# Performance work log

Hardware: AMD Instinct MI355X
Metric: run time of the kernel (lower is better)

The kernel has to match this reference:

```python
import jax, jax.numpy as jnp
import numpy as np

N, F, H, D = 4096, 512, 4, 64        # nodes, in features, heads, per-head dim
HID, OUT, NCLS, E = 1024, 256, 40, 65536  # FFN hidden, GAT dim, classes, edges
EPS = 1e-5


def _bn(x, g, b):
    # BatchNorm1d with batch statistics (training-mode math, biased variance)
    m = x.mean(axis=0)
    v = jnp.var(x, axis=0)
    return (x - m) * jax.lax.rsqrt(v + EPS) * g + b


def _ffn(x, g1, b1, W1, c1, g2, b2, W2, c2):
    x = jax.nn.gelu(_bn(x, g1, b1) @ W1.T + c1, approximate=False)
    x = jax.nn.gelu(_bn(x, g2, b2) @ W2.T + c2, approximate=False)
    return x


def setup_inputs() -> dict:
    key = jax.random.key(0)
    ks = jax.random.split(key, 12)
    nrm = lambda k, shape: jax.random.normal(k, shape, jnp.float32) * 0.05
    node_features = jax.random.normal(ks[0], (N, F), jnp.float32)
    edges = jax.random.randint(ks[1], (2, E), 0, N)
    adj = jnp.eye(N, dtype=bool)  # self loops, as in __init__
    adj = adj.at[edges[0], edges[1]].set(True)
    adj = adj.at[edges[1], edges[0]].set(True)
    return dict(
        node_features=node_features,
        pre_g1=jnp.ones(F), pre_b1=jnp.zeros(F),
        pre_W1=nrm(ks[2], (HID, F)), pre_c1=jnp.zeros(HID),
        pre_g2=jnp.ones(HID), pre_b2=jnp.zeros(HID),
        pre_W2=nrm(ks[3], (OUT, HID)), pre_c2=jnp.zeros(OUT),
        Wp=nrm(ks[4], (H * D, OUT)),           # GAT preprocess Linear, no bias
        Wa=nrm(ks[5], (2 * D,)),               # attention Linear(2d -> 1), no bias
        ln_g=jnp.ones(OUT), ln_b=jnp.zeros(OUT),
        post_g1=jnp.ones(OUT), post_b1=jnp.zeros(OUT),
        post_W1=nrm(ks[6], (HID, OUT)), post_c1=jnp.zeros(HID),
        post_g2=jnp.ones(HID), post_b2=jnp.zeros(HID),
        post_W2=nrm(ks[7], (OUT, HID)), post_c2=jnp.zeros(OUT),
        Wl=nrm(ks[8], (NCLS, OUT)), cl=jnp.zeros(NCLS),
        adjacency=adj,
        input_node_indices=jax.random.randint(ks[9], (8192,), 0, N),
    )


def reference(node_features, pre_g1, pre_b1, pre_W1, pre_c1, pre_g2, pre_b2,
              pre_W2, pre_c2, Wp, Wa, ln_g, ln_b, post_g1, post_b1, post_W1,
              post_c1, post_g2, post_b2, post_W2, post_c2, Wl, cl,
              adjacency, input_node_indices):
    # preprocess FFN: [N,F] -> [N,OUT]
    x = _ffn(node_features, pre_g1, pre_b1, pre_W1, pre_c1,
             pre_g2, pre_b2, pre_W2, pre_c2)
    # GAT layer
    xh = (x @ Wp.T).reshape(N, H, D)
    # cat([x_source, x_target]) @ Wa == x[j] . Wa[:D] + x[i] . Wa[D:]
    a_src = jnp.einsum('jhd,d->jh', xh, Wa[:D])
    a_tgt = jnp.einsum('ihd,d->ih', xh, Wa[D:])
    e = jax.nn.leaky_relu(a_src[None, :, :] + a_tgt[:, None, :],
                          negative_slope=0.2)          # [i, j, h]
    e = jnp.where(adjacency[:, :, None], e, -jnp.inf)  # masked_fill(~adj, -inf)
    att = jax.nn.softmax(e, axis=1)                    # softmax over neighbors j
    h = jnp.einsum('ijh,jhd->ihd', att, xh).reshape(N, H * D)
    # residual + LayerNorm (dropout disabled for deterministic reference)
    x = x + h
    mu = x.mean(-1, keepdims=True)
    var = jnp.var(x, axis=-1, keepdims=True)
    x = (x - mu) * jax.lax.rsqrt(var + EPS) * ln_g + ln_b
    # postprocess FFN + gather + logits
    x = _ffn(x, post_g1, post_b1, post_W1, post_c1,
             post_g2, post_b2, post_W2, post_c2)
    emb = x[input_node_indices]
    return emb @ Wl.T + cl
```

## Files before the change

### kernel.cpp

```cpp
#include <hip/hip_runtime.h>
#include <hip/hip_bf16.h>


#define NNODES 4096
#define CAP 128

typedef unsigned short u16;
typedef __attribute__((ext_vector_type(8))) short bf16x8;
typedef __attribute__((ext_vector_type(4))) float f32x4;

__device__ __forceinline__ float gelu_f(float x) {
    return 0.5f * x * (1.0f + erff(x * 0.70710678118654752f));
}
__device__ __forceinline__ u16 f2bf(float x) {
    union { float f; unsigned u; } v; v.f = x;
    unsigned r = v.u + 0x7fff + ((v.u >> 16) & 1);
    return (u16)(r >> 16);
}
__device__ __forceinline__ float bf2f(u16 b) {
    return __uint_as_float(((unsigned)b) << 16);
}
__device__ __forceinline__ void gload16(const void* g, void* l) {
    __builtin_amdgcn_global_load_lds(
        (const __attribute__((address_space(1))) unsigned int*)g,
        (__attribute__((address_space(3))) unsigned int*)l, 16, 0, 0);
}

__global__ __launch_bounds__(256) void prep_kernel(
    const unsigned char* __restrict__ adj, int* __restrict__ nbr,
    int* __restrict__ deg, const float* __restrict__ nf,
    float* __restrict__ part, u16* __restrict__ nf16)
{
    __shared__ int lists[4][CAP];
    __shared__ int cnts[4];
    __shared__ int sflag;
    const int t = threadIdx.x;
    const int wv = t >> 6, lane = t & 63;

    if (blockIdx.x >= NNODES) {
        const int bid = blockIdx.x - NNODES;
        const int r0 = bid * 32;
        const int cchunk = t & 127;
        const int rsub = t >> 7;
        float s[4] = {0.f, 0.f, 0.f, 0.f}, q[4] = {0.f, 0.f, 0.f, 0.f};
        for (int r = rsub; r < 32; r += 2) {
            float4 v = *(const float4*)(nf + (size_t)(r0 + r) * 512 + cchunk * 4);
            float vv[4] = {v.x, v.y, v.z, v.w};
            ushort4 o;
            o.x = f2bf(vv[0]); o.y = f2bf(vv[1]);
            o.z = f2bf(vv[2]); o.w = f2bf(vv[3]);
            *(ushort4*)(nf16 + (size_t)(r0 + r) * 512 + cchunk * 4) = o;
#pragma unroll
            for (int j = 0; j < 4; ++j) { s[j] += vv[j]; q[j] += vv[j] * vv[j]; }
        }
        const size_t slice = (size_t)bid * 2 + rsub;
#pragma unroll
        for (int j = 0; j < 4; ++j) {
            int c = cchunk * 4 + j;
            part[(slice * 512 + c) * 2 + 0] = s[j];
            part[(slice * 512 + c) * 2 + 1] = q[j];
        }
        return;
    }

    const int i = blockIdx.x;
    if (wv == 0) {
        bool a = adj[(size_t)lane * 4097] != 0;
        bool b = ((const unsigned int*)adj)[(size_t)lane * 4097] != 0;
        unsigned long long mA = __ballot(a);
        unsigned long long mB = __ballot(b);
        if (lane == 0) sflag = (__popcll(mA) >= __popcll(mB)) ? 0 : 1;
    }
    __syncthreads();
    int cnt = 0;
    if (sflag == 1) {
        const uint4* row = (const uint4*)((const unsigned int*)adj + (size_t)i * NNODES);
#pragma unroll
        for (int w = 0; w < 4; ++w) {
            uint4 v = row[w * 256 + t];
            unsigned wd[4] = {v.x, v.y, v.z, v.w};
#pragma unroll
            for (int j = 0; j < 4; ++j) {
                bool on = wd[j] != 0;
                unsigned long long m = __ballot(on);
                int pre = __popcll(m & ((1ull << lane) - 1ull));
                if (on && cnt + pre < CAP)
                    lists[wv][cnt + pre] = (w * 256 + t) * 4 + j;
                cnt += __popcll(m);
            }
        }
    } else {
        uint4 v = ((const uint4*)(adj + (size_t)i * NNODES))[t];
        unsigned wd[4] = {v.x, v.y, v.z, v.w};
#pragma unroll
        for (int j = 0; j < 4; ++j)
#pragma unroll
            for (int b = 0; b < 4; ++b) {
                bool on = ((wd[j] >> (8 * b)) & 0xffu) != 0;
                unsigned long long m = __ballot(on);
                int pre = __popcll(m & ((1ull << lane) - 1ull));
                if (on && cnt + pre < CAP)
                    lists[wv][cnt + pre] = t * 16 + j * 4 + b;
                cnt += __popcll(m);
            }
    }
    if (lane == 0) cnts[wv] = cnt < CAP ? cnt : CAP;
    __syncthreads();
    int offw = 0;
#pragma unroll
    for (int w2 = 0; w2 < 4; ++w2) if (w2 < wv) offw += cnts[w2];
    int myc = cnts[wv];
    for (int k = lane; k < myc; k += 64) {
        int pos = offw + k;
        if (pos < CAP) nbr[(size_t)i * CAP + pos] = lists[wv][k];
    }
    if (t == 0) {
        int tot = cnts[0] + cnts[1] + cnts[2] + cnts[3];
        deg[i] = tot < CAP ? tot : CAP;
    }
}

__global__ __launch_bounds__(256) void xln_stats(
    const float* __restrict__ X, float* __restrict__ part)
{
    const int bid = blockIdx.x;
    const int r0 = bid * 32;
    const int t = threadIdx.x;
    const int cchunk = t & 63;
    const int rsub = t >> 6;
    float s[4] = {0.f, 0.f, 0.f, 0.f}, q[4] = {0.f, 0.f, 0.f, 0.f};
    for (int r = rsub; r < 32; r += 4) {
        float4 v = *(const float4*)(X + (size_t)(r0 + r) * 256 + cchunk * 4);
        float vv[4] = {v.x, v.y, v.z, v.w};
#pragma unroll
        for (int j = 0; j < 4; ++j) { s[j] += vv[j]; q[j] += vv[j] * vv[j]; }
    }
    const size_t slice = (size_t)bid * 4 + rsub;
#pragma unroll
    for (int j = 0; j < 4; ++j) {
        int c = cchunk * 4 + j;
        part[(slice * 256 + c) * 2 + 0] = s[j];
        part[(slice * 256 + c) * 2 + 1] = q[j];
    }
}

__global__ __launch_bounds__(256) void colstats_final(
    const float* __restrict__ part, const float* __restrict__ g,
    const float* __restrict__ bt, float* __restrict__ scl,
    float* __restrict__ shf, int NB, int C)
{
    __shared__ float sred[16][17];
    __shared__ float qred[16][17];
    const int t = threadIdx.x;
    const int cs = t & 15, grp = t >> 4;
    const int c = blockIdx.x * 16 + cs;
    float s = 0.f, q = 0.f;
    for (int b = grp; b < NB; b += 16) {
        s += part[((size_t)b * C + c) * 2 + 0];
        q += part[((size_t)b * C + c) * 2 + 1];
    }
    sred[grp][cs] = s; qred[grp][cs] = q;
    __syncthreads();
    if (grp == 0) {
        float S = 0.f, Q = 0.f;
#pragma unroll
        for (int j = 0; j < 16; ++j) { S += sred[j][cs]; Q += qred[j][cs]; }
        float m = S * (1.0f / 4096.0f);
        float v = Q * (1.0f / 4096.0f) - m * m;
        float sc = g[c] * rsqrtf(v + 1e-5f);
        scl[c] = sc;
        shf[c] = bt[c] - m * sc;
    }
}

__global__ __launch_bounds__(256) void foldw_kernel(
    const float* __restrict__ W, const float* __restrict__ scl,
    const float* __restrict__ shf, const float* __restrict__ bias,
    u16* __restrict__ W16, float* __restrict__ bout, int K, int nvalid)
{
    __shared__ float red[4];
    const int n = blockIdx.x, t = threadIdx.x;
    u16* o = W16 + (size_t)n * K;
    if (n >= nvalid) {
        for (int k = t; k < K; k += 256) o[k] = 0;
        if (t == 0) bout[n] = 0.f;
        return;
    }
    const float* w = W + (size_t)n * K;
    float part = 0.f;
    for (int k = t; k < K; k += 256) {
        float wv = w[k];
        float s = scl ? scl[k] : 1.f;
        float f = shf ? shf[k] : 0.f;
        o[k] = f2bf(wv * s);
        part += wv * f;
    }
    int lane = t & 63, wv_ = t >> 6;
#pragma unroll
    for (int off = 32; off > 0; off >>= 1) part += __shfl_down(part, off);
    if (lane == 0) red[wv_] = part;
    __syncthreads();
    if (t == 0)
        bout[n] = (bias ? bias[n] : 0.f) + red[0] + red[1] + red[2] + red[3];
}

__global__ __launch_bounds__(256) void foldw2_kernel(
    const float* __restrict__ Wp, const float* __restrict__ Wl,
    const float* __restrict__ cl, u16* __restrict__ Wp16,
    u16* __restrict__ WlP16, float* __restrict__ CLP)
{
    const int n = blockIdx.x, t = threadIdx.x;
    if (n < 256) {
        Wp16[(size_t)n * 256 + t] = f2bf(Wp[(size_t)n * 256 + t]);
    } else {
        int m = n - 256;
        if (m < 40) {
            WlP16[(size_t)m * 256 + t] = f2bf(Wl[(size_t)m * 256 + t]);
            if (t == 0) CLP[m] = cl[m];
        } else {
            WlP16[(size_t)m * 256 + t] = 0;
            if (t == 0) CLP[m] = 0.f;
        }
    }
}

template<bool EPI, bool S16, bool STATS>
__global__ __launch_bounds__(256) void mfma_gemm(
    const u16* __restrict__ A, const u16* __restrict__ W,
    const float* __restrict__ bias, u16* __restrict__ C16,
    float* __restrict__ PART, int M, int N, int K)
{
    __shared__ u16 As[2][4096];
    __shared__ u16 Bs[2][4096];
    __shared__ float ep1[2][64];
    __shared__ float ep2[2][64];
    const int t = threadIdx.x;
    const int lane = t & 63, wv = t >> 6;
    const int wm = (wv >> 1) * 32, wn = (wv & 1) * 32;
    const int tile_m = blockIdx.y * 64, tile_n = blockIdx.x * 64;

    f32x4 acc[2][2];
#pragma unroll
    for (int i = 0; i < 2; ++i)
#pragma unroll
        for (int j = 0; j < 2; ++j)
#pragma unroll
            for (int e = 0; e < 4; ++e) acc[i][j][e] = 0.f;

    int srow[2], soff[2];
#pragma unroll
    for (int i = 0; i < 2; ++i) {
        int f = i * 256 + t;
        srow[i] = f >> 3;
        soff[i] = ((f & 7) ^ (srow[i] & 7)) * 8;
    }
    const int wvoff = wv * 1024;
    const int frow_a0 = wm + (lane & 15);
    const int frow_b0 = wn + (lane & 15);
    const int fk = (lane >> 4) * 16;

    const int NT = K >> 6;
    int cur = 0;

#define STAGE(B, KT)                                                         \
    {                                                                        \
        _Pragma("unroll")                                                    \
        for (int i = 0; i < 2; ++i) {                                        \
            gload16(A + (size_t)(tile_m + srow[i]) * K + (KT) * 64 + soff[i],\
                    (char*)As[B] + wvoff + i * 4096);                        \
            gload16(W + (size_t)(tile_n + srow[i]) * K + (KT) * 64 + soff[i],\
                    (char*)Bs[B] + wvoff + i * 4096);                        \
        }                                                                    \
    }

    STAGE(0, 0);
    __syncthreads();
    for (int kt = 0; kt < NT; ++kt) {
        if (kt + 1 < NT) STAGE(cur ^ 1, kt + 1);
        const char* baseA = (const char*)As[cur];
        const char* baseB = (const char*)Bs[cur];
#pragma unroll
        for (int kk = 0; kk < 2; ++kk) {
            bf16x8 a[2], b[2];
#pragma unroll
            for (int mi = 0; mi < 2; ++mi) {
                int r = frow_a0 + mi * 16;
                a[mi] = *(const bf16x8*)(baseA + r * 128 +
                        ((kk * 64 + fk) ^ ((r & 7) << 4)));
            }
#pragma unroll
            for (int ni = 0; ni < 2; ++ni) {
                int r = frow_b0 + ni * 16;
                b[ni] = *(const bf16x8*)(baseB + r * 128 +
                        ((kk * 64 + fk) ^ ((r & 7) << 4)));
            }
#pragma unroll
            for (int mi = 0; mi < 2; ++mi)
#pragma unroll
                for (int ni = 0; ni < 2; ++ni)
                    acc[mi][ni] = __builtin_amdgcn_mfma_f32_16x16x32_bf16(
                        a[mi], b[ni], acc[mi][ni], 0, 0, 0);
        }
        __syncthreads();
        cur ^= 1;
    }
#undef STAGE

    float st0 = 0.f, st1 = 0.f, sq0 = 0.f, sq1 = 0.f;
#pragma unroll
    for (int mi = 0; mi < 2; ++mi) {
#pragma unroll
        for (int ni = 0; ni < 2; ++ni) {
            int col = tile_n + wn + ni * 16 + (lane & 15);
            float bs = 0.f;
            if (EPI) bs = bias[col];
#pragma unroll
            for (int e = 0; e < 4; ++e) {
                int row = tile_m + wm + mi * 16 + ((lane >> 4) << 2) + e;
                float c = acc[mi][ni][e];
                if (EPI) c = gelu_f(c + bs);
                if (S16) C16[(size_t)row * N + col] = f2bf(c);
                if (STATS) {
                    if (ni == 0) { st0 += c; sq0 += c * c; }
                    else         { st1 += c; sq1 += c * c; }
                }
            }
        }
    }

    if (STATS) {
        float s0 = st0, s1 = st1, q0 = sq0, q1 = sq1;
        s0 += __shfl_xor(s0, 16); s0 += __shfl_xor(s0, 32);
        s1 += __shfl_xor(s1, 16); s1 += __shfl_xor(s1, 32);
        q0 += __shfl_xor(q0, 16); q0 += __shfl_xor(q0, 32);
        q1 += __shfl_xor(q1, 16); q1 += __shfl_xor(q1, 32);
        if (lane < 16) {
            ep1[wv >> 1][wn + lane] = s0;       ep2[wv >> 1][wn + lane] = q0;
            ep1[wv >> 1][wn + 16 + lane] = s1;  ep2[wv >> 1][wn + 16 + lane] = q1;
        }
        __syncthreads();
        if (t < 64) {
            PART[((size_t)blockIdx.y * N + tile_n + t) * 2 + 0] = ep1[0][t] + ep1[1][t];
            PART[((size_t)blockIdx.y * N + tile_n + t) * 2 + 1] = ep2[0][t] + ep2[1][t];
        }
    }
}

template<bool EPI, bool S16, bool ASRCF>
__global__ __launch_bounds__(512) void mfma_gemm8(
    const u16* __restrict__ A, const u16* __restrict__ W,
    const float* __restrict__ bias, u16* __restrict__ C16,
    const float* __restrict__ Wa, float* __restrict__ ASRC,
    float* __restrict__ ATGT, int M, int N, int K)
{
    __shared__ u16 As[2][4096];
    __shared__ u16 Bs[2][4096];
    __shared__ float ep1[2][64];
    __shared__ float ep2[2][64];
    const int t = threadIdx.x;
    const int lane = t & 63, wv = t >> 6;
    const int wm = (wv >> 1) * 16, wn = (wv & 1) * 32;
    const int tile_m = blockIdx.y * 64, tile_n = blockIdx.x * 64;

    f32x4 acc[2];
#pragma unroll
    for (int j = 0; j < 2; ++j)
#pragma unroll
        for (int e = 0; e < 4; ++e) acc[j][e] = 0.f;

    const int srow = t >> 3;
    const int soff = ((t & 7) ^ (srow & 7)) * 8;
    const int wvoff = wv * 1024;
    const int frow_a = wm + (lane & 15);
    const int frow_b0 = wn + (lane & 15);
    const int fk = (lane >> 4) * 16;

    const int NT = K >> 6;
    int cur = 0;

#define STAGE8(B, KT)                                                        \
    {                                                                        \
        gload16(A + (size_t)(tile_m + srow) * K + (KT) * 64 + soff,          \
                (char*)As[B] + wvoff);                                       \
        gload16(W + (size_t)(tile_n + srow) * K + (KT) * 64 + soff,          \
                (char*)Bs[B] + wvoff);                                       \
    }

    STAGE8(0, 0);
    __syncthreads();
    for (int kt = 0; kt < NT; ++kt) {
        if (kt + 1 < NT) STAGE8(cur ^ 1, kt + 1);
        const char* baseA = (const char*)As[cur];
        const char* baseB = (const char*)Bs[cur];
#pragma unroll
        for (int kk = 0; kk < 2; ++kk) {
            bf16x8 a, b[2];
            {
                int r = frow_a;
                a = *(const bf16x8*)(baseA + r * 128 +
                    ((kk * 64 + fk) ^ ((r & 7) << 4)));
            }
#pragma unroll
            for (int ni = 0; ni < 2; ++ni) {
                int r = frow_b0 + ni * 16;
                b[ni] = *(const bf16x8*)(baseB + r * 128 +
                        ((kk * 64 + fk) ^ ((r & 7) << 4)));
            }
#pragma unroll
            for (int ni = 0; ni < 2; ++ni)
                acc[ni] = __builtin_amdgcn_mfma_f32_16x16x32_bf16(
                    a, b[ni], acc[ni], 0, 0, 0);
        }
        __syncthreads();
        cur ^= 1;
    }
#undef STAGE8

#pragma unroll
    for (int ni = 0; ni < 2; ++ni) {
        int col = tile_n + wn + ni * 16 + (lane & 15);
        float bs = 0.f;
        if (EPI) bs = bias[col];
#pragma unroll
        for (int e = 0; e < 4; ++e) {
            int row = tile_m + wm + ((lane >> 4) << 2) + e;
            float c = acc[ni][e];
            if (EPI) c = gelu_f(c + bs);
            if (S16) C16[(size_t)row * N + col] = f2bf(c);
        }
    }

    if (ASRCF) {
        const int cl = lane & 15;
        float ws0 = Wa[wn + cl],      ws1 = Wa[wn + 16 + cl];
        float wt0 = Wa[64 + wn + cl], wt1 = Wa[64 + wn + 16 + cl];
#pragma unroll
        for (int e = 0; e < 4; ++e) {
            float vs = acc[0][e] * ws0 + acc[1][e] * ws1;
            float vt = acc[0][e] * wt0 + acc[1][e] * wt1;
#pragma unroll
            for (int off = 1; off < 16; off <<= 1) {
                vs += __shfl_xor(vs, off);
                vt += __shfl_xor(vt, off);
            }
            if (cl == 0) {
                int row = wm + ((lane >> 4) << 2) + e;
                ep1[wv & 1][row] = vs;
                ep2[wv & 1][row] = vt;
            }
        }
        __syncthreads();
        if (t < 64) {
            int h = blockIdx.x;
            ASRC[(size_t)(tile_m + t) * 4 + h] = ep1[0][t] + ep1[1][t];
            ATGT[(size_t)(tile_m + t) * 4 + h] = ep2[0][t] + ep2[1][t];
        }
    }
}

__global__ __launch_bounds__(512) void logits_mfma(
    const u16* __restrict__ xf16, const int* __restrict__ idxs,
    const u16* __restrict__ WlP, const float* __restrict__ clP,
    float* __restrict__ out)
{
    __shared__ u16 As[2][4096];
    __shared__ u16 Bs[2][4096];
    const int t = threadIdx.x;
    const int lane = t & 63, wv = t >> 6;
    const int wm = (wv >> 1) * 16, wn = (wv & 1) * 32;
    const int tile_m = blockIdx.x * 64;

    f32x4 acc[2];
#pragma unroll
    for (int j = 0; j < 2; ++j)
#pragma unroll
        for (int e = 0; e < 4; ++e) acc[j][e] = 0.f;

    const int srow = t >> 3;
    const int soff = ((t & 7) ^ (srow & 7)) * 8;
    const int gr = idxs[tile_m + srow];
    const int wvoff = wv * 1024;
    const int frow_a = wm + (lane & 15);
    const int frow_b0 = wn + (lane & 15);
    const int fk = (lane >> 4) * 16;

#define LSTAGE8(B, KT)                                                       \
    {                                                                        \
        gload16(xf16 + (size_t)gr * 256 + (KT) * 64 + soff,                  \
                (char*)As[B] + wvoff);                                       \
        gload16(WlP + (size_t)srow * 256 + (KT) * 64 + soff,                 \
                (char*)Bs[B] + wvoff);                                       \
    }

    int cur = 0;
    LSTAGE8(0, 0);
    __syncthreads();
#pragma unroll
    for (int kt = 0; kt < 4; ++kt) {
        if (kt + 1 < 4) LSTAGE8(cur ^ 1, kt + 1);
        const char* baseA = (const char*)As[cur];
        const char* baseB = (const char*)Bs[cur];
#pragma unroll
        for (int kk = 0; kk < 2; ++kk) {
            bf16x8 a, b[2];
            {
                int r = frow_a;
                a = *(const bf16x8*)(baseA + r * 128 +
                    ((kk * 64 + fk) ^ ((r & 7) << 4)));
            }
#pragma unroll
            for (int ni = 0; ni < 2; ++ni) {
                int r = frow_b0 + ni * 16;
                b[ni] = *(const bf16x8*)(baseB + r * 128 +
                        ((kk * 64 + fk) ^ ((r & 7) << 4)));
            }
#pragma unroll
            for (int ni = 0; ni < 2; ++ni)
                acc[ni] = __builtin_amdgcn_mfma_f32_16x16x32_bf16(
                    a, b[ni], acc[ni], 0, 0, 0);
        }
        __syncthreads();
        cur ^= 1;
    }
#undef LSTAGE8

#pragma unroll
    for (int ni = 0; ni < 2; ++ni) {
        int col = wn + ni * 16 + (lane & 15);
        if (col < 40) {
            float bs = clP[col];
#pragma unroll
            for (int e = 0; e < 4; ++e) {
                int row = tile_m + wm + ((lane >> 4) << 2) + e;
                out[(size_t)row * 40 + col] = acc[ni][e] + bs;
            }
        }
    }
}

__global__ __launch_bounds__(256) void attn_ln_kernel(
    const u16* __restrict__ xh, const u16* __restrict__ x0,
    const float* __restrict__ asrc, const float* __restrict__ atgt,
    const int* __restrict__ nbr, const int* __restrict__ deg_,
    const float* __restrict__ ln_g, const float* __restrict__ ln_b,
    float* __restrict__ xln32, u16* __restrict__ xln16)
{
    __shared__ float att[CAP * 4];
    __shared__ int nb[CAP];
    __shared__ float red[8];
    const int i = blockIdx.x;
    const int t = threadIdx.x;
    const int wv = t >> 6, lane = t & 63;
    const int dg = deg_[i];

    for (int k = t; k < dg; k += 256) nb[k] = nbr[(size_t)i * CAP + k];
    __syncthreads();

    for (int idx = t; idx < dg * 4; idx += 256) {
        int k = idx >> 2, h = idx & 3;
        float e = asrc[nb[k] * 4 + h] + atgt[i * 4 + h];
        att[idx] = e > 0.f ? e : 0.2f * e;
    }
    __syncthreads();

    {
        const int h = wv;
        float m = -1e30f;
        for (int k = lane; k < dg; k += 64) m = fmaxf(m, att[k * 4 + h]);
#pragma unroll
        for (int off = 32; off > 0; off >>= 1) m = fmaxf(m, __shfl_xor(m, off));
        float s = 0.f;
        for (int k = lane; k < dg; k += 64) s += expf(att[k * 4 + h] - m);
#pragma unroll
        for (int off = 32; off > 0; off >>= 1) s += __shfl_xor(s, off);
        float inv = 1.0f / s;
        for (int k = lane; k < dg; k += 64)
            att[k * 4 + h] = expf(att[k * 4 + h] - m) * inv;
    }

    const int h = wv;
    float acc = 0.f;
    int k = 0;
    for (; k + 4 <= dg; k += 4) {
        float a0 = att[(k + 0) * 4 + h], v0 = bf2f(xh[(size_t)nb[k + 0] * 256 + t]);
        float a1 = att[(k + 1) * 4 + h], v1 = bf2f(xh[(size_t)nb[k + 1] * 256 + t]);
        float a2 = att[(k + 2) * 4 + h], v2 = bf2f(xh[(size_t)nb[k + 2] * 256 + t]);
        float a3 = att[(k + 3) * 4 + h], v3 = bf2f(xh[(size_t)nb[k + 3] * 256 + t]);
        acc = fmaf(a0, v0, acc); acc = fmaf(a1, v1, acc);
        acc = fmaf(a2, v2, acc); acc = fmaf(a3, v3, acc);
    }
    for (; k < dg; ++k)
        acc = fmaf(att[k * 4 + h], bf2f(xh[(size_t)nb[k] * 256 + t]), acc);

    float v = bf2f(x0[(size_t)i * 256 + t]) + acc;
    float s = v, q = v * v;
#pragma unroll
    for (int off = 32; off > 0; off >>= 1) {
        s += __shfl_xor(s, off);
        q += __shfl_xor(q, off);
    }
    if (lane == 0) { red[wv] = s; red[4 + wv] = q; }
    __syncthreads();
    float S = red[0] + red[1] + red[2] + red[3];
    float Q = red[4] + red[5] + red[6] + red[7];
    float mu = S * (1.0f / 256.0f);
    float var = Q * (1.0f / 256.0f) - mu * mu;
    float y = (v - mu) * rsqrtf(var + 1e-5f) * ln_g[t] + ln_b[t];
    xln32[(size_t)i * 256 + t] = y;
    xln16[(size_t)i * 256 + t] = f2bf(y);
}

extern "C" void kernel_launch(void* const* d_in, const int* in_sizes, int n_in,
                              void* d_out, int out_size, void* d_ws, size_t ws_size,
                              hipStream_t stream)
{
    const float* nf      = (const float*)d_in[0];
    const float* pre_g1  = (const float*)d_in[1];
    const float* pre_b1  = (const float*)d_in[2];
    const float* pre_W1  = (const float*)d_in[3];
    const float* pre_c1  = (const float*)d_in[4];
    const float* pre_g2  = (const float*)d_in[5];
    const float* pre_b2  = (const float*)d_in[6];
    const float* pre_W2  = (const float*)d_in[7];
    const float* pre_c2  = (const float*)d_in[8];
    const float* Wp      = (const float*)d_in[9];
    const float* Wa      = (const float*)d_in[10];
    const float* ln_g    = (const float*)d_in[11];
    const float* ln_b    = (const float*)d_in[12];
    const float* post_g1 = (const float*)d_in[13];
    const float* post_b1 = (const float*)d_in[14];
    const float* post_W1 = (const float*)d_in[15];
    const float* post_c1 = (const float*)d_in[16];
    const float* post_g2 = (const float*)d_in[17];
    const float* post_b2 = (const float*)d_in[18];
    const float* post_W2 = (const float*)d_in[19];
    const float* post_c2 = (const float*)d_in[20];
    const float* Wl      = (const float*)d_in[21];
    const float* cl      = (const float*)d_in[22];
    const unsigned char* adj = (const unsigned char*)d_in[23];
    const int* idxs      = (const int*)d_in[24];
    float* out = (float*)d_out;

    size_t off = 0;
    char* base = (char*)d_ws;
    auto carve = [&](size_t bytes) {
        void* p = base + off;
        off += (bytes + 255) & ~(size_t)255;
        return p;
    };
    u16*   Y16   = (u16*)  carve((size_t)4096 * 1024 * 2);
    u16*   NF16  = (u16*)  carve((size_t)4096 * 512 * 2);
    u16*   X016  = (u16*)  carve((size_t)4096 * 256 * 2);
    u16*   XH16  = (u16*)  carve((size_t)4096 * 256 * 2);
    float* XLN32 = (float*)carve((size_t)4096 * 256 * 4);
    u16*   XLN16 = (u16*)  carve((size_t)4096 * 256 * 2);
    u16*   XF16  = (u16*)  carve((size_t)4096 * 256 * 2);
    u16*   W1_16 = (u16*)  carve((size_t)1024 * 512 * 2);
    u16*   W2_16 = (u16*)  carve((size_t)256 * 1024 * 2);
    u16*   Wp16  = (u16*)  carve((size_t)256 * 256 * 2);
    u16*   W3_16 = (u16*)  carve((size_t)1024 * 256 * 2);
    u16*   W4_16 = (u16*)  carve((size_t)256 * 1024 * 2);
    u16*   WlP16 = (u16*)  carve((size_t)64 * 256 * 2);
    float* B1    = (float*)carve(1024 * 4);
    float* B2    = (float*)carve(256 * 4);
    float* B3    = (float*)carve(1024 * 4);
    float* B4    = (float*)carve(256 * 4);
    float* CLP   = (float*)carve(64 * 4);
    int*   NBR   = (int*)  carve((size_t)4096 * CAP * 4);
    int*   DEG   = (int*)  carve((size_t)4096 * 4);
    float* ASRC  = (float*)carve((size_t)4096 * 4 * 4);
    float* ATGT  = (float*)carve((size_t)4096 * 4 * 4);
    float* PART  = (float*)carve((size_t)512 * 512 * 2 * 4);
    float* SCL1  = (float*)carve(512 * 4);
    float* SHF1  = (float*)carve(512 * 4);
    float* SCL2  = (float*)carve(1024 * 4);
    float* SHF2  = (float*)carve(1024 * 4);
    float* SCL3  = (float*)carve(256 * 4);
    float* SHF3  = (float*)carve(256 * 4);
    float* SCL4  = (float*)carve(1024 * 4);
    float* SHF4  = (float*)carve(1024 * 4);
    (void)ws_size; (void)n_in; (void)in_sizes; (void)out_size;

    prep_kernel<<<NNODES + 128, 256, 0, stream>>>(adj, NBR, DEG, nf, PART, NF16);

    colstats_final<<<512 / 16, 256, 0, stream>>>(PART, pre_g1, pre_b1, SCL1, SHF1, 256, 512);
    foldw_kernel<<<1024, 256, 0, stream>>>(pre_W1, SCL1, SHF1, pre_c1, W1_16, B1, 512, 1024);
    mfma_gemm<true, true, true><<<dim3(16, 64), 256, 0, stream>>>(
        NF16, W1_16, B1, Y16, PART, 4096, 1024, 512);

    colstats_final<<<1024 / 16, 256, 0, stream>>>(PART, pre_g2, pre_b2, SCL2, SHF2, 64, 1024);
    foldw_kernel<<<256, 256, 0, stream>>>(pre_W2, SCL2, SHF2, pre_c2, W2_16, B2, 1024, 256);
    mfma_gemm8<true, true, false><<<dim3(4, 64), 512, 0, stream>>>(
        Y16, W2_16, B2, X016, nullptr, nullptr, nullptr, 4096, 256, 1024);

    foldw2_kernel<<<320, 256, 0, stream>>>(Wp, Wl, cl, Wp16, WlP16, CLP);

    mfma_gemm8<false, true, true><<<dim3(4, 64), 512, 0, stream>>>(
        X016, Wp16, nullptr, XH16, Wa, ASRC, ATGT, 4096, 256, 256);

    attn_ln_kernel<<<4096, 256, 0, stream>>>(XH16, X016, ASRC, ATGT, NBR, DEG,
                                             ln_g, ln_b, XLN32, XLN16);

    xln_stats<<<128, 256, 0, stream>>>(XLN32, PART);
    colstats_final<<<256 / 16, 256, 0, stream>>>(PART, post_g1, post_b1, SCL3, SHF3, 512, 256);
    foldw_kernel<<<1024, 256, 0, stream>>>(post_W1, SCL3, SHF3, post_c1, W3_16, B3, 256, 1024);
    mfma_gemm<true, true, true><<<dim3(16, 64), 256, 0, stream>>>(
        XLN16, W3_16, B3, Y16, PART, 4096, 1024, 256);

    colstats_final<<<1024 / 16, 256, 0, stream>>>(PART, post_g2, post_b2, SCL4, SHF4, 64, 1024);
    foldw_kernel<<<256, 256, 0, stream>>>(post_W2, SCL4, SHF4, post_c2, W4_16, B4, 1024, 256);
    mfma_gemm8<true, true, false><<<dim3(4, 64), 512, 0, stream>>>(
        Y16, W4_16, B4, XF16, nullptr, nullptr, nullptr, 4096, 256, 1024);

    logits_mfma<<<128, 512, 0, stream>>>(XF16, idxs, WlP16, CLP, out);
}
```

Measured before the change: 139.7 us.

## Split K across wave halves in 512-thread GEMMs and fold weight cast into prep

The 512-thread GEMM and logits kernels now give each group of four waves half of the K range, with 32x32 warp tiles, and reduce the two partial accumulators through shared memory before the epilogue. Each wave issues more MFMAs per LDS fragment load and the K loop is half as long. The cost is doubled shared memory, an extra LDS reduction pass and a barrier. Separately, the Wp/Wl bf16 conversion kernel is folded into extra blocks of the prep kernel to remove one launch.

```diff
diff --git a/kernel.cpp b/kernel.cpp
--- a/kernel.cpp
+++ b/kernel.cpp
@@ -29,13 +29,33 @@
 __global__ __launch_bounds__(256) void prep_kernel(
     const unsigned char* __restrict__ adj, int* __restrict__ nbr,
     int* __restrict__ deg, const float* __restrict__ nf,
-    float* __restrict__ part, u16* __restrict__ nf16)
+    float* __restrict__ part, u16* __restrict__ nf16,
+    const float* __restrict__ Wp, const float* __restrict__ Wl,
+    const float* __restrict__ cl, u16* __restrict__ Wp16,
+    u16* __restrict__ WlP16, float* __restrict__ CLP)
 {
     __shared__ int lists[4][CAP];
     __shared__ int cnts[4];
     __shared__ int sflag;
     const int t = threadIdx.x;
     const int wv = t >> 6, lane = t & 63;
+
+    if (blockIdx.x >= NNODES + 128) {
+        const int n = blockIdx.x - (NNODES + 128);
+        if (n < 256) {
+            Wp16[(size_t)n * 256 + t] = f2bf(Wp[(size_t)n * 256 + t]);
+        } else {
+            int m = n - 256;
+            if (m < 40) {
+                WlP16[(size_t)m * 256 + t] = f2bf(Wl[(size_t)m * 256 + t]);
+                if (t == 0) CLP[m] = cl[m];
+            } else {
+                WlP16[(size_t)m * 256 + t] = 0;
+                if (t == 0) CLP[m] = 0.f;
+            }
+        }
+        return;
+    }
 
     if (blockIdx.x >= NNODES) {
         const int bid = blockIdx.x - NNODES;
@@ -204,26 +224,6 @@
         bout[n] = (bias ? bias[n] : 0.f) + red[0] + red[1] + red[2] + red[3];
 }
 
-__global__ __launch_bounds__(256) void foldw2_kernel(
-    const float* __restrict__ Wp, const float* __restrict__ Wl,
-    const float* __restrict__ cl, u16* __restrict__ Wp16,
-    u16* __restrict__ WlP16, float* __restrict__ CLP)
-{
-    const int n = blockIdx.x, t = threadIdx.x;
-    if (n < 256) {
-        Wp16[(size_t)n * 256 + t] = f2bf(Wp[(size_t)n * 256 + t]);
-    } else {
-        int m = n - 256;
-        if (m < 40) {
-            WlP16[(size_t)m * 256 + t] = f2bf(Wl[(size_t)m * 256 + t]);
-            if (t == 0) CLP[m] = cl[m];
-        } else {
-            WlP16[(size_t)m * 256 + t] = 0;
-            if (t == 0) CLP[m] = 0.f;
-        }
-    }
-}
-
 template<bool EPI, bool S16, bool STATS>
 __global__ __launch_bounds__(256) void mfma_gemm(
     const u16* __restrict__ A, const u16* __restrict__ W,
@@ -353,52 +353,69 @@
     const float* __restrict__ Wa, float* __restrict__ ASRC,
     float* __restrict__ ATGT, int M, int N, int K)
 {
-    __shared__ u16 As[2][4096];
-    __shared__ u16 Bs[2][4096];
+    __shared__ u16 As[2][2][4096];
+    __shared__ u16 Bs[2][2][4096];
     __shared__ float ep1[2][64];
     __shared__ float ep2[2][64];
     const int t = threadIdx.x;
     const int lane = t & 63, wv = t >> 6;
-    const int wm = (wv >> 1) * 16, wn = (wv & 1) * 32;
+    const int kh = wv >> 2;
+    const int wl = wv & 3;
+    const int wm = (wl >> 1) * 32, wn = (wl & 1) * 32;
     const int tile_m = blockIdx.y * 64, tile_n = blockIdx.x * 64;
 
-    f32x4 acc[2];
-#pragma unroll
-    for (int j = 0; j < 2; ++j)
-#pragma unroll
-        for (int e = 0; e < 4; ++e) acc[j][e] = 0.f;
-
-    const int srow = t >> 3;
-    const int soff = ((t & 7) ^ (srow & 7)) * 8;
-    const int wvoff = wv * 1024;
-    const int frow_a = wm + (lane & 15);
+    f32x4 acc[2][2];
+#pragma unroll
+    for (int i = 0; i < 2; ++i)
+#pragma unroll
+        for (int j = 0; j < 2; ++j)
+#pragma unroll
+            for (int e = 0; e < 4; ++e) acc[i][j][e] = 0.f;
+
+    const int ht = t & 255;
+    int srow[2], soff[2];
+#pragma unroll
+    for (int i = 0; i < 2; ++i) {
+        int f = i * 256 + ht;
+        srow[i] = f >> 3;
+        soff[i] = ((f & 7) ^ (srow[i] & 7)) * 8;
+    }
+    const int wvoff = wl * 1024;
+    const int frow_a0 = wm + (lane & 15);
     const int frow_b0 = wn + (lane & 15);
     const int fk = (lane >> 4) * 16;
 
-    const int NT = K >> 6;
+    const int NTh = (K >> 6) >> 1;
+    const int kbase = kh * NTh;
     int cur = 0;
 
 #define STAGE8(B, KT)                                                        \
     {                                                                        \
-        gload16(A + (size_t)(tile_m + srow) * K + (KT) * 64 + soff,          \
-                (char*)As[B] + wvoff);                                       \
-        gload16(W + (size_t)(tile_n + srow) * K + (KT) * 64 + soff,          \
-                (char*)Bs[B] + wvoff);                                       \
+        _Pragma("unroll")                                                    \
+        for (int i = 0; i < 2; ++i) {                                        \
+            gload16(A + (size_t)(tile_m + srow[i]) * K + (kbase + (KT)) * 64 \
+                        + soff[i],                                           \
+                    (char*)As[B][kh] + wvoff + i * 4096);                    \
+            gload16(W + (size_t)(tile_n + srow[i]) * K + (kbase + (KT)) * 64 \
+                        + soff[i],                                           \
+                    (char*)Bs[B][kh] + wvoff + i * 4096);                    \
+        }                                                                    \
     }
 
     STAGE8(0, 0);
     __syncthreads();
-    for (int kt = 0; kt < NT; ++kt) {
-        if (kt + 1 < NT) STAGE8(cur ^ 1, kt + 1);
-        const char* baseA = (const char*)As[cur];
-        const char* baseB = (const char*)Bs[cur];
+    for (int kt = 0; kt < NTh; ++kt) {
+        if (kt + 1 < NTh) STAGE8(cur ^ 1, kt + 1);
+        const char* baseA = (const char*)As[cur][kh];
+        const char* baseB = (const char*)Bs[cur][kh];
 #pragma unroll
         for (int kk = 0; kk < 2; ++kk) {
-            bf16x8 a, b[2];
-            {
-                int r = frow_a;
-                a = *(const bf16x8*)(baseA + r * 128 +
-                    ((kk * 64 + fk) ^ ((r & 7) << 4)));
+            bf16x8 a[2], b[2];
+#pragma unroll
+            for (int mi = 0; mi < 2; ++mi) {
+                int r = frow_a0 + mi * 16;
+                a[mi] = *(const bf16x8*)(baseA + r * 128 +
+                        ((kk * 64 + fk) ^ ((r & 7) << 4)));
             }
 #pragma unroll
             for (int ni = 0; ni < 2; ++ni) {
@@ -407,53 +424,85 @@
                         ((kk * 64 + fk) ^ ((r & 7) << 4)));
             }
 #pragma unroll
-            for (int ni = 0; ni < 2; ++ni)
-                acc[ni] = __builtin_amdgcn_mfma_f32_16x16x32_bf16(
-                    a, b[ni], acc[ni], 0, 0, 0);
+            for (int mi = 0; mi < 2; ++mi)
+#pragma unroll
+                for (int ni = 0; ni < 2; ++ni)
+                    acc[mi][ni] = __builtin_amdgcn_mfma_f32_16x16x32_bf16(
+                        a[mi], b[ni], acc[mi][ni], 0, 0, 0);
         }
         __syncthreads();
         cur ^= 1;
     }
 #undef STAGE8
 
-#pragma unroll
-    for (int ni = 0; ni < 2; ++ni) {
-        int col = tile_n + wn + ni * 16 + (lane & 15);
-        float bs = 0.f;
-        if (EPI) bs = bias[col];
-#pragma unroll
-        for (int e = 0; e < 4; ++e) {
-            int row = tile_m + wm + ((lane >> 4) << 2) + e;
-            float c = acc[ni][e];
-            if (EPI) c = gelu_f(c + bs);
-            if (S16) C16[(size_t)row * N + col] = f2bf(c);
+    float* cb = (float*)&As[0][0][0];
+    if (kh == 1) {
+#pragma unroll
+        for (int mi = 0; mi < 2; ++mi)
+#pragma unroll
+            for (int ni = 0; ni < 2; ++ni)
+#pragma unroll
+                for (int e = 0; e < 4; ++e)
+                    cb[wl * 1024 + lane * 16 + (mi * 2 + ni) * 4 + e] =
+                        acc[mi][ni][e];
+    }
+    __syncthreads();
+    if (kh == 0) {
+#pragma unroll
+        for (int mi = 0; mi < 2; ++mi)
+#pragma unroll
+            for (int ni = 0; ni < 2; ++ni)
+#pragma unroll
+                for (int e = 0; e < 4; ++e)
+                    acc[mi][ni][e] +=
+                        cb[wl * 1024 + lane * 16 + (mi * 2 + ni) * 4 + e];
+
+#pragma unroll
+        for (int mi = 0; mi < 2; ++mi) {
+#pragma unroll
+            for (int ni = 0; ni < 2; ++ni) {
+                int col = tile_n + wn + ni * 16 + (lane & 15);
+                float bs = 0.f;
+                if (EPI) bs = bias[col];
+#pragma unroll
+                for (int e = 0; e < 4; ++e) {
+                    int row = tile_m + wm + mi * 16 + ((lane >> 4) << 2) + e;
+                    float c = acc[mi][ni][e];
+                    if (EPI) c = gelu_f(c + bs);
+                    if (S16) C16[(size_t)row * N + col] = f2bf(c);
+                }
+            }
         }
     }
 
     if (ASRCF) {
-        const int cl = lane & 15;
-        float ws0 = Wa[wn + cl],      ws1 = Wa[wn + 16 + cl];
-        float wt0 = Wa[64 + wn + cl], wt1 = Wa[64 + wn + 16 + cl];
-#pragma unroll
-        for (int e = 0; e < 4; ++e) {
-            float vs = acc[0][e] * ws0 + acc[1][e] * ws1;
-            float vt = acc[0][e] * wt0 + acc[1][e] * wt1;
-#pragma unroll
-            for (int off = 1; off < 16; off <<= 1) {
-                vs += __shfl_xor(vs, off);
-                vt += __shfl_xor(vt, off);
-            }
-            if (cl == 0) {
-                int row = wm + ((lane >> 4) << 2) + e;
-                ep1[wv & 1][row] = vs;
-                ep2[wv & 1][row] = vt;
-            }
+        if (kh == 0) {
+            const int cl = lane & 15;
+            float ws0 = Wa[wn + cl],      ws1 = Wa[wn + 16 + cl];
+            float wt0 = Wa[64 + wn + cl], wt1 = Wa[64 + wn + 16 + cl];
+#pragma unroll
+            for (int mi = 0; mi < 2; ++mi)
+#pragma unroll
+                for (int e = 0; e < 4; ++e) {
+                    float vs = acc[mi][0][e] * ws0 + acc[mi][1][e] * ws1;
+                    float vt = acc[mi][0][e] * wt0 + acc[mi][1][e] * wt1;
+#pragma unroll
+                    for (int off = 1; off < 16; off <<= 1) {
+                        vs += __shfl_xor(vs, off);
+                        vt += __shfl_xor(vt, off);
+                    }
+                    if (cl == 0) {
+                        int row = wm + mi * 16 + ((lane >> 4) << 2) + e;
+                        ep1[wl & 1][row] = vs;
+                        ep2[wl & 1][row] = vt;
+                    }
+                }
         }
         __syncthreads();
         if (t < 64) {
-            int h = blockIdx.x;
-            ASRC[(size_t)(tile_m + t) * 4 + h] = ep1[0][t] + ep1[1][t];
-            ATGT[(size_t)(tile_m + t) * 4 + h] = ep2[0][t] + ep2[1][t];
+            int head = blockIdx.x;
+            ASRC[(size_t)(tile_m + t) * 4 + head] = ep1[0][t] + ep1[1][t];
+            ATGT[(size_t)(tile_m + t) * 4 + head] = ep2[0][t] + ep2[1][t];
         }
     }
 }
@@ -463,50 +512,67 @@
     const u16* __restrict__ WlP, const float* __restrict__ clP,
     float* __restrict__ out)
 {
-    __shared__ u16 As[2][4096];
-    __shared__ u16 Bs[2][4096];
+    __shared__ u16 As[2][2][4096];
+    __shared__ u16 Bs[2][2][4096];
     const int t = threadIdx.x;
     const int lane = t & 63, wv = t >> 6;
-    const int wm = (wv >> 1) * 16, wn = (wv & 1) * 32;
+    const int kh = wv >> 2;
+    const int wl = wv & 3;
+    const int wm = (wl >> 1) * 32, wn = (wl & 1) * 32;
     const int tile_m = blockIdx.x * 64;
 
-    f32x4 acc[2];
-#pragma unroll
-    for (int j = 0; j < 2; ++j)
-#pragma unroll
-        for (int e = 0; e < 4; ++e) acc[j][e] = 0.f;
-
-    const int srow = t >> 3;
-    const int soff = ((t & 7) ^ (srow & 7)) * 8;
-    const int gr = idxs[tile_m + srow];
-    const int wvoff = wv * 1024;
-    const int frow_a = wm + (lane & 15);
+    f32x4 acc[2][2];
+#pragma unroll
+    for (int i = 0; i < 2; ++i)
+#pragma unroll
+        for (int j = 0; j < 2; ++j)
+#pragma unroll
+            for (int e = 0; e < 4; ++e) acc[i][j][e] = 0.f;
+
+    const int ht = t & 255;
+    int srow[2], soff[2], gr[2];
+#pragma unroll
+    for (int i = 0; i < 2; ++i) {
+        int f = i * 256 + ht;
+        srow[i] = f >> 3;
+        soff[i] = ((f & 7) ^ (srow[i] & 7)) * 8;
+        gr[i] = idxs[tile_m + srow[i]];
+    }
+    const int wvoff = wl * 1024;
+    const int frow_a0 = wm + (lane & 15);
     const int frow_b0 = wn + (lane & 15);
     const int fk = (lane >> 4) * 16;
+    const int kbase = kh * 2;
 
 #define LSTAGE8(B, KT)                                                       \
     {                                                                        \
-        gload16(xf16 + (size_t)gr * 256 + (KT) * 64 + soff,                  \
-                (char*)As[B] + wvoff);                                       \
-        gload16(WlP + (size_t)srow * 256 + (KT) * 64 + soff,                 \
-                (char*)Bs[B] + wvoff);                                       \
+        _Pragma("unroll")                                                    \
+        for (int i = 0; i < 2; ++i) {                                        \
+            gload16(xf16 + (size_t)gr[i] * 256 + (kbase + (KT)) * 64         \
+                        + soff[i],                                           \
+                    (char*)As[B][kh] + wvoff + i * 4096);                    \
+            gload16(WlP + (size_t)srow[i] * 256 + (kbase + (KT)) * 64        \
+                        + soff[i],                                           \
+                    (char*)Bs[B][kh] + wvoff + i * 4096);                    \
+        }                                                                    \
     }
 
     int cur = 0;
     LSTAGE8(0, 0);
     __syncthreads();
 #pragma unroll
-    for (int kt = 0; kt < 4; ++kt) {
-        if (kt + 1 < 4) LSTAGE8(cur ^ 1, kt + 1);
-        const char* baseA = (const char*)As[cur];
-        const char* baseB = (const char*)Bs[cur];
+    for (int kt = 0; kt < 2; ++kt) {
+        if (kt + 1 < 2) LSTAGE8(cur ^ 1, kt + 1);
+        const char* baseA = (const char*)As[cur][kh];
+        const char* baseB = (const char*)Bs[cur][kh];
 #pragma unroll
         for (int kk = 0; kk < 2; ++kk) {
-            bf16x8 a, b[2];
-            {
-                int r = frow_a;
-                a = *(const bf16x8*)(baseA + r * 128 +
-                    ((kk * 64 + fk) ^ ((r & 7) << 4)));
+            bf16x8 a[2], b[2];
+#pragma unroll
+            for (int mi = 0; mi < 2; ++mi) {
+                int r = frow_a0 + mi * 16;
+                a[mi] = *(const bf16x8*)(baseA + r * 128 +
+                        ((kk * 64 + fk) ^ ((r & 7) << 4)));
             }
 #pragma unroll
             for (int ni = 0; ni < 2; ++ni) {
@@ -515,24 +581,47 @@
                         ((kk * 64 + fk) ^ ((r & 7) << 4)));
             }
 #pragma unroll
-            for (int ni = 0; ni < 2; ++ni)
-                acc[ni] = __builtin_amdgcn_mfma_f32_16x16x32_bf16(
-                    a, b[ni], acc[ni], 0, 0, 0);
+            for (int mi = 0; mi < 2; ++mi)
+#pragma unroll
+                for (int ni = 0; ni < 2; ++ni)
+                    acc[mi][ni] = __builtin_amdgcn_mfma_f32_16x16x32_bf16(
+                        a[mi], b[ni], acc[mi][ni], 0, 0, 0);
         }
         __syncthreads();
         cur ^= 1;
     }
 #undef LSTAGE8
 
-#pragma unroll
-    for (int ni = 0; ni < 2; ++ni) {
-        int col = wn + ni * 16 + (lane & 15);
-        if (col < 40) {
-            float bs = clP[col];
-#pragma unroll
-            for (int e = 0; e < 4; ++e) {
-                int row = tile_m + wm + ((lane >> 4) << 2) + e;
-                out[(size_t)row * 40 + col] = acc[ni][e] + bs;
+    float* cb = (float*)&As[0][0][0];
+    if (kh == 1) {
+#pragma unroll
+        for (int mi = 0; mi < 2; ++mi)
+#pragma unroll
+            for (int ni = 0; ni < 2; ++ni)
+#pragma unroll
+                for (int e = 0; e < 4; ++e)
+                    cb[wl * 1024 + lane * 16 + (mi * 2 + ni) * 4 + e] =
+                        acc[mi][ni][e];
+    }
+    __syncthreads();
+    if (kh == 0) {
+#pragma unroll
+        for (int mi = 0; mi < 2; ++mi) {
+#pragma unroll
+            for (int ni = 0; ni < 2; ++ni) {
+                int col = wn + ni * 16 + (lane & 15);
+                float cbsum0 = cb[wl * 1024 + lane * 16 + (mi * 2 + ni) * 4];
+                (void)cbsum0;
+                if (col < 40) {
+                    float bs = clP[col];
+#pragma unroll
+                    for (int e = 0; e < 4; ++e) {
+                        int row = tile_m + wm + mi * 16 + ((lane >> 4) << 2) + e;
+                        float c = acc[mi][ni][e] +
+                            cb[wl * 1024 + lane * 16 + (mi * 2 + ni) * 4 + e];
+                        out[(size_t)row * 40 + col] = c + bs;
+                    }
+                }
             }
         }
     }
@@ -681,7 +770,8 @@
     float* SHF4  = (float*)carve(1024 * 4);
     (void)ws_size; (void)n_in; (void)in_sizes; (void)out_size;
 
-    prep_kernel<<<NNODES + 128, 256, 0, stream>>>(adj, NBR, DEG, nf, PART, NF16);
+    prep_kernel<<<NNODES + 128 + 320, 256, 0, stream>>>(
+        adj, NBR, DEG, nf, PART, NF16, Wp, Wl, cl, Wp16, WlP16, CLP);
 
     colstats_final<<<512 / 16, 256, 0, stream>>>(PART, pre_g1, pre_b1, SCL1, SHF1, 256, 512);
     foldw_kernel<<<1024, 256, 0, stream>>>(pre_W1, SCL1, SHF1, pre_c1, W1_16, B1, 512, 1024);
@@ -692,8 +782,6 @@
     foldw_kernel<<<256, 256, 0, stream>>>(pre_W2, SCL2, SHF2, pre_c2, W2_16, B2, 1024, 256);
     mfma_gemm8<true, true, false><<<dim3(4, 64), 512, 0, stream>>>(
         Y16, W2_16, B2, X016, nullptr, nullptr, nullptr, 4096, 256, 1024);
-
-    foldw2_kernel<<<320, 256, 0, stream>>>(Wp, Wl, cl, Wp16, WlP16, CLP);
 
     mfma_gemm8<false, true, true><<<dim3(4, 64), 512, 0, stream>>>(
         X016, Wp16, nullptr, XH16, Wa, ASRC, ATGT, 4096, 256, 256);
```

Result: faster. 135.6 us (-2.9%).
